# Optimization experiments

Measured on AMD Instinct MI355X. Metric: run time of the kernel, lower is better.

Reference implementation:

```python
import jax, jax.numpy as jnp
import numpy as np

B, F, R, P, C = 2048, 64, 32, 16, 128  # batch, nfeature(dsym), nrole, npattern, dcontext
TAU = 2.0  # posn_attender sharpness


def setup_inputs() -> dict:
    key = jax.random.key(0)
    ks = jax.random.split(key, 16)
    w = lambda k, shape, s=0.05: jax.random.normal(k, shape, jnp.float32) * s
    z = lambda shape: jnp.zeros(shape, jnp.float32)
    return {
        "form": jax.random.normal(ks[0], (B, F, R), jnp.float32),
        "context": jax.random.normal(ks[1], (B, C), jnp.float32),
        "mod_W": w(ks[2], (C, P * 6)), "mod_b": z((P * 6,)),
        "wch_W": w(ks[3], (C, P * F)), "wch_b": z((P * F,)),
        "wdl_W": w(ks[4], (C, P)), "wdl_b": z((P,)),
        "wep_W": w(ks[5], (C, P * 4)), "wep_b": z((P * 4,)),
        "vch_W": w(ks[6], (C, P * F)), "vch_b": z((P * F,)),
        "vep_W": w(ks[7], (C, P * F * 4)), "vep_b": z((P * F * 4,)),
        "wnc_W": w(ks[8], (C, F)), "wnc_b": z((F,)),
        "wnd_W": w(ks[9], (C, 1)), "wnd_b": z((1,)),
        "wne_W": w(ks[10], (C, 1)), "wne_b": z((1,)),
        "m_W": w(ks[11], (3, C, P * F)), "m_Wb": z((3, P * F)),
        "mb_W": w(ks[12], (3, C, P)), "mb_b": z((3, P)),
    }


def _forward(form, context, mod_W, mod_b, wch_W, wch_b, wdl_W, wdl_b,
             wep_W, wep_b, vch_W, vch_b, vep_W, vep_b,
             wnc_W, wnc_b, wnd_W, wnd_b, wne_W, wne_b,
             m_W, m_Wb, mb_W, mb_b):
    nb = form.shape[0]
    lin = lambda W, b: context @ W + b

    # context-conditioned rule weights
    mod = jax.nn.softmax(lin(mod_W, mod_b).reshape(nb, P, 6), axis=-1)
    w_chng = mod[..., 0:1] * lin(wch_W, wch_b).reshape(nb, P, F)
    w_deln = mod[..., 1:2] * lin(wdl_W, wdl_b).reshape(nb, P, 1)
    w_epen = mod[..., 2:] * lin(wep_W, wep_b).reshape(nb, P, 4)
    v_chng = lin(vch_W, vch_b).reshape(nb, P, F)
    v_epen = lin(vep_W, vep_b).reshape(nb, P, F, 4)
    w_nochng = jnp.exp(lin(wnc_W, wnc_b))   # (B, F)
    w_nodeln = jnp.exp(lin(wnd_W, wnd_b))   # (B, 1)
    w_noepen = jnp.exp(lin(wne_W, wne_b))   # (B, 1)

    # Matcher3: trigram (prev, cur, next) feature matching; log-prob summed then exp'd
    prev = jnp.pad(form[:, :, :-1], ((0, 0), (0, 0), (1, 0)))
    nxt = jnp.pad(form[:, :, 1:], ((0, 0), (0, 0), (0, 1)))
    forms3 = jnp.stack([prev, form, nxt], 0)                                   # (3,B,F,R)
    Wk = (jnp.einsum('bc,kcn->kbn', context, m_W) + m_Wb[:, None, :]).reshape(3, nb, P, F)
    bk = jnp.einsum('bc,kcp->kbp', context, mb_W) + mb_b[:, None, :]
    score = jnp.einsum('kbpf,kbfr->kbpr', Wk, forms3) + bk[..., None]
    match = jnp.exp(jnp.sum(jax.nn.log_sigmoid(score), axis=0))                # (B,P,R)

    positions = jnp.arange(R, dtype=form.dtype)

    def posn_attn(posn):  # (B,1) soft position -> (B,R) radial-basis attention
        return jax.nn.softmax(-TAU * (posn - positions[None, :]) ** 2, axis=-1)

    def bind(out, x, attn):  # soft write symbol x at attended role
        a = attn[:, None, :]
        return out * (1.0 - a) + x[:, :, None] * a

    def epen(out, posn, match_i, we_p, ve_p):
        we = match_i * we_p                                                    # (B,P)
        p = jax.nn.sigmoid(jnp.sum(we, 1, keepdims=True) - w_noepen)           # (B,1)
        v = jnp.sum(jax.nn.relu(we)[..., None] * ve_p, 1)                      # (B,F)
        out_ = bind(out, v, posn_attn(posn))
        out = p[..., None] * out_ + (1.0 - p[..., None]) * out
        return out, posn + p

    def step(carry, x):
        out, posn = carry
        sym_i, match_i = x  # (B,F), (B,P)
        # epenthesis before
        out, posn = epen(out, posn, match_i, w_epen[..., 0], v_epen[..., 0])
        # feature change + deletion
        wc = match_i[..., None] * w_chng                                       # (B,P,F)
        p_chng = jax.nn.sigmoid(jnp.sum(wc, 1) - w_nochng)                     # (B,F)
        vc = jnp.sum(jax.nn.relu(wc) * v_chng, 1)                              # (B,F)
        sym = sym_i + p_chng * (vc - sym_i)
        out_ = bind(out, sym, posn_attn(posn))
        wd = match_i[..., None] * w_deln                                       # (B,P,1)
        p_deln = jax.nn.sigmoid(jnp.sum(wd, 1) - w_nodeln)                     # (B,1)
        out = (1.0 - p_deln[..., None]) * out_ + p_deln[..., None] * out
        posn = posn + (1.0 - p_deln)
        # epenthesis after
        out, posn = epen(out, posn, match_i, w_epen[..., 2], v_epen[..., 2])
        return (out, posn), None

    carry0 = (jnp.zeros((nb, F, R), form.dtype), jnp.zeros((nb, 1), form.dtype))
    xs = (jnp.moveaxis(form, 2, 0), jnp.moveaxis(match, 2, 0))
    (out, _), _ = jax.lax.scan(step, carry0, xs)
    return out


def reference(form, context, mod_W, mod_b, wch_W, wch_b, wdl_W, wdl_b,
              wep_W, wep_b, vch_W, vch_b, vep_W, vep_b,
              wnc_W, wnc_b, wnd_W, wnd_b, wne_W, wne_b,
              m_W, m_Wb, mb_W, mb_b):
    return _forward(form, context, mod_W, mod_b, wch_W, wch_b, wdl_W, wdl_b,
                    wep_W, wep_b, vch_W, vch_b, vep_W, vep_b,
                    wnc_W, wnc_b, wnd_W, wnd_b, wne_W, wne_b,
                    m_W, m_Wb, mb_W, mb_b)
```

## Files before the change

kernel.cpp:

```cpp
#include <hip/hip_runtime.h>

#define B_ 2048
#define YS2 7168
#define NTILES 448

typedef unsigned short u16;
typedef unsigned int   u32;
typedef __attribute__((ext_vector_type(2))) float v2f;
typedef __attribute__((ext_vector_type(8))) short bf16x8;
typedef __attribute__((ext_vector_type(4))) float f32x4;

__device__ __forceinline__ float bfu(u16 u) {
    u32 i = ((u32)u) << 16; float f; __builtin_memcpy(&f, &i, 4); return f;
}
__device__ __forceinline__ u16 f2bf(float v) {
    u32 iv; __builtin_memcpy(&iv, &v, 4);
    u32 r = (iv + 0x7fffu + ((iv >> 16) & 1u)) >> 16;
    return (u16)r;
}
__device__ __forceinline__ float sigm(float x) { return 1.f / (1.f + __expf(-x)); }
__device__ __forceinline__ float lsg(float x) {
    return fminf(x, 0.f) - log1pf(__expf(-fabsf(x)));
}

template<bool F32> __device__ __forceinline__ float LD(const void* p, int e) {
    if (F32) return ((const float*)p)[e];
    return bfu(((const u16*)p)[e]);
}
template<bool F32> __device__ __forceinline__ float2 LD2(const void* p, int e) {
    if (F32) { const float* q = (const float*)p; return make_float2(q[e], q[e + 1]); }
    u32 w = ((const u32*)p)[e >> 1];
    u32 lo = w << 16, hi = w & 0xffff0000u; float a, b;
    __builtin_memcpy(&a, &lo, 4); __builtin_memcpy(&b, &hi, 4);
    return make_float2(a, b);
}
template<bool F32> __device__ __forceinline__ float4 LD4(const void* p, int e) {
    if (F32) return ((const float4*)p)[e >> 2];
    uint2 w = ((const uint2*)p)[e >> 2];
    u32 a0 = w.x << 16, a1 = w.x & 0xffff0000u, a2 = w.y << 16, a3 = w.y & 0xffff0000u;
    float f0, f1, f2, f3;
    __builtin_memcpy(&f0, &a0, 4); __builtin_memcpy(&f1, &a1, 4);
    __builtin_memcpy(&f2, &a2, 4); __builtin_memcpy(&f3, &a3, 4);
    return make_float4(f0, f1, f2, f3);
}
template<bool F32> __device__ __forceinline__ void ST(void* p, int e, float v) {
    if (F32) ((float*)p)[e] = v; else ((u16*)p)[e] = f2bf(v);
}

struct Args {
    const void *form, *ctx;
    const void *mod_W, *mod_b, *wch_W, *wch_b, *wdl_W, *wdl_b, *wep_W, *wep_b;
    const void *vch_W, *vch_b, *vep_W, *vep_b;
    const void *wnc_W, *wnc_b, *wnd_W, *wnd_b, *wne_W, *wne_b;
    const void *m_W, *m_Wb, *mb_W, *mb_b;
    void* outp;
};

__device__ __forceinline__ int probe_is_f32(const void* ctx, int t, int* flag_s) {
    if (t == 0) {
        int sane = 0;
        const u16* q = (const u16*)ctx;
        for (int i = 0; i < 64; ++i) {
            u16 u = q[2 * i];
            int ex = (u >> 7) & 0xFF;
            sane += (u == 0 || (ex >= 112 && ex <= 143)) ? 1 : 0;
        }
        *flag_s = (sane < 32) ? 1 : 0;
    }
    __syncthreads();
    return *flag_s;
}

__device__ __forceinline__ void split_bf16(float x, u16& hi, u16& lo) {
    hi = f2bf(x);
    lo = f2bf(x - bfu(hi));
}


template<bool F32>
__device__ void packw_body(int g, const Args& A, u16* Bpack, float* bcat) {
    int l  = g & 63;
    int kb = (g >> 6) & 3;
    int h  = (g >> 8) & 1;
    int T  = g >> 9;
    int n  = T * 16 + (l & 15);
    int k0 = kb * 32 + (l >> 4) * 8;

    const void* p; int off, st;
    if (n < 1024)      { p = A.wch_W; off = n;           st = 1024; }
    else if (n < 2048) { p = A.vch_W; off = n - 1024;    st = 1024; }
    else if (n < 4096) { int i = n - 2048; int col = 4 * (i >> 1) + 2 * (i & 1);
                         p = A.vep_W; off = col;         st = 4096; }
    else               { int i = n - 4096; int kk = i >> 10, j2 = i & 1023;
                         p = A.m_W;  off = kk * 131072 + j2; st = 1024; }

    u16 out[8];
    #pragma unroll
    for (int j = 0; j < 8; ++j) {
        float w = LD<F32>(p, off + (k0 + j) * st);
        u16 whi, wlo; split_bf16(w, whi, wlo);
        out[j] = h ? wlo : whi;
    }
    *(uint4*)(Bpack + (size_t)g * 8) = *(const uint4*)out;

    if (h == 0 && kb == 0 && l < 16) {
        float bb;
        if (n < 1024)      bb = LD<F32>(A.wch_b, n);
        else if (n < 2048) bb = LD<F32>(A.vch_b, n - 1024);
        else if (n < 4096) { int i = n - 2048; bb = LD<F32>(A.vep_b, 4 * (i >> 1) + 2 * (i & 1)); }
        else               { int i = n - 4096; bb = LD<F32>(A.m_Wb, (i >> 10) * 1024 + (i & 1023)); }
        bcat[n] = bb;
    }
}

__global__ __launch_bounds__(256) void packw_kernel(Args A, u16* Bpack, float* bcat) {
    __shared__ int dt_s;
    const int t = threadIdx.x;
    int isf32 = probe_is_f32(A.ctx, t, &dt_s);
    int g = blockIdx.x * 256 + t;
    if (isf32) packw_body<true>(g, A, Bpack, bcat);
    else       packw_body<false>(g, A, Bpack, bcat);
}

template<bool F32>
__device__ void packa_body(int g, const Args& A, u16* Apack) {
    int l  = g & 63;
    int kb = (g >> 6) & 3;
    int h  = (g >> 8) & 1;
    int M  = g >> 9;
    int m  = M * 16 + (l & 15);
    int k0 = kb * 32 + (l >> 4) * 8;

    u16 out[8];
    float4 x = LD4<F32>(A.ctx, m * 128 + k0);
    float4 y = LD4<F32>(A.ctx, m * 128 + k0 + 4);
    float v[8] = {x.x, x.y, x.z, x.w, y.x, y.y, y.z, y.w};
    #pragma unroll
    for (int j = 0; j < 8; ++j) {
        u16 whi, wlo; split_bf16(v[j], whi, wlo);
        out[j] = h ? wlo : whi;
    }
    *(uint4*)(Apack + (size_t)g * 8) = *(const uint4*)out;
}

__global__ __launch_bounds__(256) void packa_kernel(Args A, u16* Apack) {
    __shared__ int dt_s;
    const int t = threadIdx.x;
    int isf32 = probe_is_f32(A.ctx, t, &dt_s);
    int g = blockIdx.x * 256 + t;
    if (isf32) packa_body<true>(g, A, Apack);
    else       packa_body<false>(g, A, Apack);
}

__global__ __launch_bounds__(256) void gemm_mfma_kernel(
    const u16* __restrict__ Apack, const u16* __restrict__ Bpack,
    const float* __restrict__ bcat, float* __restrict__ Y) {
    __shared__ __align__(16) u16 Astage[4096];

    const int t  = threadIdx.x;
    const int l  = t & 63;
    const int w  = t >> 6;
    const int Mt = blockIdx.x & 127;
    const int nb = blockIdx.x >> 7;

    {
        const uint4* Ap4 = (const uint4*)(Apack + (size_t)Mt * 4096);
        uint4* As4 = (uint4*)Astage;
        As4[t] = Ap4[t];
        As4[t + 256] = Ap4[t + 256];
    }
    __syncthreads();

    bf16x8 ahi[4], alo[4];
    #pragma unroll
    for (int kb = 0; kb < 4; ++kb) {
        ahi[kb] = *(const bf16x8*)(Astage + ((0 * 4 + kb) * 64 + l) * 8);
        alo[kb] = *(const bf16x8*)(Astage + ((1 * 4 + kb) * 64 + l) * 8);
    }

    const int Tbase = nb * 16 + w * 4;
    const int row0  = Mt * 16 + (l >> 4) * 4;
    const int ncol  = l & 15;

    #pragma unroll
    for (int T = 0; T < 4; ++T) {
        const u16* Bb = Bpack + (size_t)(Tbase + T) * 4096;
        bf16x8 bhi[4], blo[4];
        #pragma unroll
        for (int kb = 0; kb < 4; ++kb) {
            bhi[kb] = *(const bf16x8*)(Bb + ((0 * 4 + kb) * 64 + l) * 8);
            blo[kb] = *(const bf16x8*)(Bb + ((1 * 4 + kb) * 64 + l) * 8);
        }
        f32x4 d = {0.f, 0.f, 0.f, 0.f};
        #pragma unroll
        for (int kb = 0; kb < 4; ++kb) {
            d = __builtin_amdgcn_mfma_f32_16x16x32_bf16(ahi[kb], bhi[kb], d, 0, 0, 0);
            d = __builtin_amdgcn_mfma_f32_16x16x32_bf16(ahi[kb], blo[kb], d, 0, 0, 0);
            d = __builtin_amdgcn_mfma_f32_16x16x32_bf16(alo[kb], bhi[kb], d, 0, 0, 0);
        }
        int n = (Tbase + T) * 16 + ncol;
        float bv = bcat[n];
        #pragma unroll
        for (int i = 0; i < 4; ++i) {
            Y[(size_t)(row0 + i) * YS2 + n] = d[i] + bv;
        }
    }
}

struct __align__(16) ScanSmem {
    float U[6144];
    float V[3072];
    float match_s[512];
    float wnc_s[64];
    float wep0_s[16], wep2_s[16], wdl_s[16];
    float coef_s[96];
    float sc_s[2];
};

template<bool F32>
__device__ void scan_body(ScanSmem& S, int t, int b, const Args& A, const float* __restrict__ Y) {
    float* Wk_s   = S.U;
    float* bk_s   = S.U + 3072;
    float* modl   = S.U + 3120;
    float* form_s = S.U + 3312;
    float* ctx_s  = S.U + 5424;
    float* xtab   = S.U;
    float* wch_s  = S.V;
    float* vch_s  = S.V + 1024;
    float* rlI    = S.V + 2048;
    float* gtab   = S.V;

    const float* Yr = Y + (size_t)b * YS2;
    const float4* Y4 = (const float4*)Yr;

    const int f_own = t & 63;
    const int fq    = t >> 6;

    const float2* vep2p = (const float2*)(Yr + 2048);
    v2f vepf[16];
    #pragma unroll
    for (int p = 0; p < 16; ++p) {
        float2 v = vep2p[p * 64 + f_own];
        vepf[p].x = v.x; vepf[p].y = v.y;
    }

    {
        int e0 = b * 2048 + t * 8;
        float4 x = LD4<F32>(A.form, e0);
        float4 y = LD4<F32>(A.form, e0 + 4);
        int f = t >> 2, r0 = (t & 3) * 8;
        float* dst = form_s + f * 33 + r0;
        dst[0] = x.x; dst[1] = x.y; dst[2] = x.z; dst[3] = x.w;
        dst[4] = y.x; dst[5] = y.y; dst[6] = y.z; dst[7] = y.w;
    }
    if (t < 32) {
        float4 v = LD4<F32>(A.ctx, b * 128 + 4 * t);
        *(float4*)&ctx_s[4 * t] = v;
    }
    for (int i = t; i < 768; i += 256) ((float4*)Wk_s)[i] = Y4[1024 + i];
    ((float4*)wch_s)[t] = Y4[t];
    ((float4*)vch_s)[t] = Y4[256 + t];
    __syncthreads();

    if (t < 96) {
        float a = LD<F32>(A.mod_b, t);
        for (int c = 0; c < 128; ++c) a += ctx_s[c] * LD<F32>(A.mod_W, c * 96 + t);
        modl[t] = a;
    } else if (t < 144) {
        int i = t - 96; int k = i >> 4, p = i & 15;
        float a = LD<F32>(A.mb_b, k * 16 + p);
        for (int c = 0; c < 128; ++c) a += ctx_s[c] * LD<F32>(A.mb_W, (k * 128 + c) * 16 + p);
        bk_s[i] = a;
    } else if (t < 208) {
        int f = t - 144;
        float a = LD<F32>(A.wnc_b, f);
        for (int c = 0; c < 128; ++c) a += ctx_s[c] * LD<F32>(A.wnc_W, c * 64 + f);
        S.wnc_s[f] = __expf(a);
    } else if (t < 224) {
        int p = t - 208;
        float a0 = LD<F32>(A.wep_b, 4 * p), a2 = LD<F32>(A.wep_b, 4 * p + 2);
        for (int c = 0; c < 128; ++c) {
            float cv = ctx_s[c];
            a0 += cv * LD<F32>(A.wep_W, c * 64 + 4 * p);
            a2 += cv * LD<F32>(A.wep_W, c * 64 + 4 * p + 2);
        }
        S.wep0_s[p] = a0; S.wep2_s[p] = a2;
    } else if (t < 240) {
        int p = t - 224;
        float a = LD<F32>(A.wdl_b, p);
        for (int c = 0; c < 128; ++c) a += ctx_s[c] * LD<F32>(A.wdl_W, c * 16 + p);
        S.wdl_s[p] = a;
    } else if (t < 242) {
        const void* W  = (t == 240) ? A.wnd_W : A.wne_W;
        const void* bb = (t == 240) ? A.wnd_b : A.wne_b;
        float a = LD<F32>(bb, 0);
        for (int c = 0; c < 128; ++c) a += ctx_s[c] * LD<F32>(W, c);
        S.sc_s[t - 240] = __expf(a);
    }
    __syncthreads();

    if (t < 16) {
        float v[6]; float mx = -1e30f;
        #pragma unroll
        for (int j = 0; j < 6; ++j) { v[j] = modl[t * 6 + j]; mx = fmaxf(mx, v[j]); }
        float s = 0.f;
        #pragma unroll
        for (int j = 0; j < 6; ++j) { v[j] = __expf(v[j] - mx); s += v[j]; }
        float inv = 1.f / s;
        #pragma unroll
        for (int j = 0; j < 6; ++j) modl[t * 6 + j] = v[j] * inv;
    }
    __syncthreads();

    if (t < 16) {
        S.wep0_s[t] *= modl[t * 6 + 2];
        S.wep2_s[t] *= modl[t * 6 + 4];
        S.wdl_s[t]  *= modl[t * 6 + 1];
    }
    for (int i = t; i < 1024; i += 256) wch_s[i] *= modl[(i >> 6) * 6];

    const int my_r = t & 31;
    #pragma unroll 1
    for (int it = 0; it < 2; ++it) {
        int idx = t + 256 * it;
        int p = idx >> 5, r = idx & 31;
        float s0 = bk_s[p], s1 = bk_s[16 + p], s2 = bk_s[32 + p];
        const float4* w0 = (const float4*)(Wk_s + p * 64);
        const float4* w1 = (const float4*)(Wk_s + (16 + p) * 64);
        const float4* w2 = (const float4*)(Wk_s + (32 + p) * 64);
        for (int f4 = 0; f4 < 16; ++f4) {
            float a0[4], a1[4], a2[4];
            *(float4*)a0 = w0[f4]; *(float4*)a1 = w1[f4]; *(float4*)a2 = w2[f4];
            #pragma unroll
            for (int j = 0; j < 4; ++j) {
                int f = f4 * 4 + j;
                float f0 = form_s[f * 33 + r];
                float fm = __shfl_up(f0, 1, 32);   if (r == 0)  fm = 0.f;
                float fp = __shfl_down(f0, 1, 32); if (r == 31) fp = 0.f;
                s0 += a0[j] * fm; s1 += a1[j] * f0; s2 += a2[j] * fp;
            }
        }
        S.match_s[p * 32 + r] = __expf(lsg(s0) + lsg(s1) + lsg(s2));
    }
    __syncthreads();

    if (t < 96) {
        int sub = t >> 5, r = t & 31;
        const float* w = (sub == 0) ? S.wep0_s : (sub == 1) ? S.wdl_s : S.wep2_s;
        float s = 0.f;
        for (int p = 0; p < 16; ++p) s += S.match_s[p * 32 + r] * w[p];
        float cf;
        if (sub == 1) cf = 1.f - sigm(s - S.sc_s[0]);
        else          cf = sigm(s - S.sc_s[1]);
        S.coef_s[sub * 32 + r] = cf;
    }
    for (int i = t; i < 512; i += 256) {
        int p = i >> 5, r = i & 31;
        float m = S.match_s[p * 32 + r];
        rlI[2 * i]     = fmaxf(m * S.wep0_s[p], 0.f);
        rlI[2 * i + 1] = fmaxf(m * S.wep2_s[p], 0.f);
    }
    float wchf[16], vchf[16];
    #pragma unroll
    for (int p = 0; p < 16; ++p) {
        wchf[p] = wch_s[p * 64 + f_own];
        vchf[p] = vch_s[p * 64 + f_own];
    }
    const float wncf = S.wnc_s[f_own];
    float si_r[8];
    #pragma unroll
    for (int j = 0; j < 8; ++j) si_r[j] = form_s[f_own * 33 + fq * 8 + j];
    __syncthreads();

    #pragma unroll 1
    for (int j = 0; j < 8; ++j) {
        int rs = fq * 8 + j;
        v2f v02; v02.x = 0.f; v02.y = 0.f;
        float sum = 0.f, vs1 = 0.f;
        const v2f* rlp = (const v2f*)(rlI + 2 * rs);
        #pragma unroll
        for (int p = 0; p < 16; ++p) {
            v2f rl = rlp[p * 32];
            v02 += rl * vepf[p];
            float m = S.match_s[p * 32 + rs];
            float wc = m * wchf[p];
            sum += wc;
            vs1 += fmaxf(wc, 0.f) * vchf[p];
        }
        float pch = sigm(sum - wncf);
        float si  = si_r[j];
        xtab[0 * 2048 + rs * 64 + f_own] = v02.x;
        xtab[1 * 2048 + rs * 64 + f_own] = si + pch * (vs1 - si);
        xtab[2 * 2048 + rs * 64 + f_own] = v02.y;
    }
    __syncthreads();

    float* ck_s  = S.match_s;
    float* pos_s = S.match_s + 128;
    if (t < 96) ck_s[t] = S.coef_s[(t % 3) * 32 + (t / 3)];
    __syncthreads();
    if (t < 64) {
        float a = ck_s[t];
        float a0 = a;
        #pragma unroll
        for (int d = 1; d < 64; d <<= 1) { float v = __shfl_up(a, d, 64); if (t >= d) a += v; }
        pos_s[t] = a - a0;
        float carry = __shfl(a, 63, 64);
        float b2 = (t < 32) ? ck_s[64 + t] : 0.f;
        float c2 = b2;
        #pragma unroll
        for (int d = 1; d < 32; d <<= 1) { float v = __shfl_up(c2, d, 32); if ((t & 31) >= d) c2 += v; }
        if (t < 32) pos_s[64 + t] = carry + c2 - b2;
    }
    __syncthreads();

    #pragma unroll 1
    for (int i = 0; i < 12; ++i) {
        int idx = t + 256 * i;
        int k = idx >> 5, r = idx & 31;
        float posn = pos_s[k];
        float pc = fminf(posn, 31.f);
        float ci = floorf(pc + 0.5f);
        float dmin = posn - ci;
        float dd = posn - (float)r;
        float eo = __expf(-2.f * (dd * dd - dmin * dmin));
        float Z = eo;
        Z += __shfl_xor(Z, 1, 32);
        Z += __shfl_xor(Z, 2, 32);
        Z += __shfl_xor(Z, 4, 32);
        Z += __shfl_xor(Z, 8, 32);
        Z += __shfl_xor(Z, 16, 32);
        gtab[idx] = ck_s[k] * eo / Z;
    }
    __syncthreads();

    const int fgrp = t >> 5;
    v2f o01, o23, o45, o67;
    o01 = 0.f; o23 = 0.f; o45 = 0.f; o67 = 0.f;
    #pragma unroll 1
    for (int rs = 0; rs < 32; ++rs) {
        #pragma unroll
        for (int sub = 0; sub < 3; ++sub) {
            float g = gtab[(rs * 3 + sub) * 32 + my_r];
            v2f gv; gv.x = g; gv.y = g;
            const float4* xb = (const float4*)(xtab + sub * 2048 + rs * 64 + fgrp * 8);
            float4 xa = xb[0], xc = xb[1];
            v2f x01, x23, x45, x67;
            x01.x = xa.x; x01.y = xa.y; x23.x = xa.z; x23.y = xa.w;
            x45.x = xc.x; x45.y = xc.y; x67.x = xc.z; x67.y = xc.w;
            o01 += gv * (x01 - o01);
            o23 += gv * (x23 - o23);
            o45 += gv * (x45 - o45);
            o67 += gv * (x67 - o67);
        }
    }

    float oreg[8] = {o01.x, o01.y, o23.x, o23.y, o45.x, o45.y, o67.x, o67.y};
    #pragma unroll
    for (int i = 0; i < 8; ++i) {
        ST<F32>(A.outp, b * 2048 + (fgrp * 8 + i) * 32 + my_r, oreg[i]);
    }
}

__global__ __launch_bounds__(256) void scan_kernel(Args A, const float* Y) {
    __shared__ ScanSmem S;
    __shared__ int dt_s;
    const int t = threadIdx.x, b = blockIdx.x;
    int isf32 = probe_is_f32(A.ctx, t, &dt_s);
    if (isf32) scan_body<true>(S, t, b, A, Y);
    else       scan_body<false>(S, t, b, A, Y);
}

struct Smem {
    float U[6144];
    float form_s[64 * 33];
    float match_s[512];
    float wch_s[1024];
    float vch_s[1024];
    float vep0_s[1024];
    float vep2_s[1024];
    float wep0_s[16], wep2_s[16], wdl_s[16];
    float wnc_s[64];
    float sc_s[2];
    float ssum_s[96];
};

template<bool F32>
__device__ void mono_body(Smem& S, int t, int b, const Args& A) {
    float* c_s  = S.U;
    float* modl = S.U + 128;
    float* Wk_s = S.U + 224;
    float* bk_s = S.U + 3344;
    float* xtab = S.U;

    if (t < 128) c_s[t] = LD<F32>(A.ctx, b * 128 + t);
    {
        int e0 = b * 2048 + t * 8;
        float4 x = LD4<F32>(A.form, e0);
        float4 y = LD4<F32>(A.form, e0 + 4);
        int f = t >> 2, r0 = (t & 3) * 8;
        float* dst = S.form_s + f * 33 + r0;
        dst[0] = x.x; dst[1] = x.y; dst[2] = x.z; dst[3] = x.w;
        dst[4] = y.x; dst[5] = y.y; dst[6] = y.z; dst[7] = y.w;
    }
    __syncthreads();
    if (t < 96) {
        float a = LD<F32>(A.mod_b, t);
        for (int cc = 0; cc < 128; ++cc) a += c_s[cc] * LD<F32>(A.mod_W, cc * 96 + t);
        modl[t] = a;
    }
    __syncthreads();
    if (t < 16) {
        float v[6]; float mx = -1e30f;
        #pragma unroll
        for (int j = 0; j < 6; ++j) { v[j] = modl[t * 6 + j]; mx = fmaxf(mx, v[j]); }
        float s = 0.f;
        #pragma unroll
        for (int j = 0; j < 6; ++j) { v[j] = __expf(v[j] - mx); s += v[j]; }
        float inv = 1.f / s;
        #pragma unroll
        for (int j = 0; j < 6; ++j) modl[t * 6 + j] = v[j] * inv;
    }
    __syncthreads();
    for (int j = t; j < 512; j += 256) {
        int n0 = j * 2;
        float2 bb = LD2<F32>(A.wch_b, n0);
        float a0 = bb.x, a1 = bb.y;
        for (int cc = 0; cc < 128; ++cc) {
            float2 w = LD2<F32>(A.wch_W, cc * 1024 + n0); float cv = c_s[cc];
            a0 += cv * w.x; a1 += cv * w.y;
        }
        int p = n0 >> 6; float sc = modl[p * 6 + 0];
        S.wch_s[n0] = sc * a0; S.wch_s[n0 + 1] = sc * a1;
    }
    for (int j = t; j < 512; j += 256) {
        int n0 = j * 2;
        float2 bb = LD2<F32>(A.vch_b, n0);
        float a0 = bb.x, a1 = bb.y;
        for (int cc = 0; cc < 128; ++cc) {
            float2 w = LD2<F32>(A.vch_W, cc * 1024 + n0); float cv = c_s[cc];
            a0 += cv * w.x; a1 += cv * w.y;
        }
        S.vch_s[n0] = a0; S.vch_s[n0 + 1] = a1;
    }
    for (int u = t; u < 1024; u += 256) {
        int n0 = u * 4;
        float4 bb = LD4<F32>(A.vep_b, n0);
        float a0 = bb.x, a2 = bb.z;
        for (int cc = 0; cc < 128; ++cc) {
            float4 w = LD4<F32>(A.vep_W, cc * 4096 + n0); float cv = c_s[cc];
            a0 += cv * w.x; a2 += cv * w.z;
        }
        S.vep0_s[u] = a0; S.vep2_s[u] = a2;
    }
    for (int j = t; j < 1536; j += 256) {
        int k  = j >> 9;
        int jj = j & 511;
        int n0 = jj * 2;
        float2 bb = LD2<F32>(A.m_Wb, k * 1024 + n0);
        float a0 = bb.x, a1 = bb.y;
        for (int cc = 0; cc < 128; ++cc) {
            float2 w = LD2<F32>(A.m_W, (k * 128 + cc) * 1024 + n0); float cv = c_s[cc];
            a0 += cv * w.x; a1 += cv * w.y;
        }
        int p = n0 >> 6, f = n0 & 63;
        Wk_s[(k * 16 + p) * 65 + f]     = a0;
        Wk_s[(k * 16 + p) * 65 + f + 1] = a1;
    }
    if (t < 16) {
        int n0 = t * 4;
        float4 bb = LD4<F32>(A.wep_b, n0);
        float a0 = bb.x, a2 = bb.z;
        for (int cc = 0; cc < 128; ++cc) {
            float4 w = LD4<F32>(A.wep_W, cc * 64 + n0); float cv = c_s[cc];
            a0 += cv * w.x; a2 += cv * w.z;
        }
        S.wep0_s[t] = modl[t * 6 + 2] * a0;
        S.wep2_s[t] = modl[t * 6 + 4] * a2;
    } else if (t < 32) {
        int p = t - 16;
        float a = LD<F32>(A.wdl_b, p);
        for (int cc = 0; cc < 128; ++cc) a += c_s[cc] * LD<F32>(A.wdl_W, cc * 16 + p);
        S.wdl_s[p] = modl[p * 6 + 1] * a;
    } else if (t < 96) {
        int f = t - 32;
        float a = LD<F32>(A.wnc_b, f);
        for (int cc = 0; cc < 128; ++cc) a += c_s[cc] * LD<F32>(A.wnc_W, cc * 64 + f);
        S.wnc_s[f] = __expf(a);
    } else if (t < 98) {
        const void* W  = (t == 96) ? A.wnd_W : A.wne_W;
        const void* bb = (t == 96) ? A.wnd_b : A.wne_b;
        float a = LD<F32>(bb, 0);
        for (int cc = 0; cc < 128; ++cc) a += c_s[cc] * LD<F32>(W, cc);
        S.sc_s[t - 96] = __expf(a);
    } else if (t < 146) {
        int i = t - 98;
        int k = i >> 4, p = i & 15;
        float a = LD<F32>(A.mb_b, k * 16 + p);
        for (int cc = 0; cc < 128; ++cc) a += c_s[cc] * LD<F32>(A.mb_W, (k * 128 + cc) * 16 + p);
        bk_s[i] = a;
    }
    __syncthreads();
    for (int idx = t; idx < 512; idx += 256) {
        int p = idx >> 5, r = idx & 31;
        float s0 = bk_s[p], s1 = bk_s[16 + p], s2 = bk_s[32 + p];
        const float* w0 = Wk_s + p * 65;
        const float* w1 = Wk_s + (16 + p) * 65;
        const float* w2 = Wk_s + (32 + p) * 65;
        for (int f = 0; f < 64; ++f) {
            const float* fr = S.form_s + f * 33 + r;
            float fm1 = (r > 0)  ? fr[-1] : 0.f;
            float f0  = fr[0];
            float fp1 = (r < 31) ? fr[1]  : 0.f;
            s0 += w0[f] * fm1; s1 += w1[f] * f0; s2 += w2[f] * fp1;
        }
        S.match_s[p * 32 + r] = __expf(lsg(s0) + lsg(s1) + lsg(s2));
    }
    __syncthreads();
    if (t < 96) {
        int which = t >> 5, r = t & 31;
        const float* w = (which == 0) ? S.wep0_s : (which == 1) ? S.wep2_s : S.wdl_s;
        float s = 0.f;
        for (int p = 0; p < 16; ++p) s += S.match_s[p * 32 + r] * w[p];
        S.ssum_s[which * 32 + r] = s;
    }
    #pragma unroll 1
    for (int q = 0; q < 24; ++q) {
        int idx = t + 256 * q;
        int sub = idx >> 11;
        int rs  = (idx >> 6) & 31;
        int f   = idx & 63;
        float x;
        if (sub == 1) {
            float sum = 0.f, vs = 0.f;
            for (int p = 0; p < 16; ++p) {
                float wc = S.match_s[p * 32 + rs] * S.wch_s[p * 64 + f];
                sum += wc;
                vs  += fmaxf(wc, 0.f) * S.vch_s[p * 64 + f];
            }
            float pch = sigm(sum - S.wnc_s[f]);
            float si  = S.form_s[f * 33 + rs];
            x = si + pch * (vs - si);
        } else {
            const float* wep = (sub == 0) ? S.wep0_s : S.wep2_s;
            const float* vep = (sub == 0) ? S.vep0_s : S.vep2_s;
            float vs = 0.f;
            for (int p = 0; p < 16; ++p) {
                float w = S.match_s[p * 32 + rs] * wep[p];
                vs += fmaxf(w, 0.f) * vep[p * 64 + f];
            }
            x = vs;
        }
        xtab[idx] = x;
    }
    __syncthreads();
    const int my_r = t & 31;
    const int fgrp = t >> 5;
    float oreg[8];
    #pragma unroll
    for (int i = 0; i < 8; ++i) oreg[i] = 0.f;
    float posn = 0.f;
    const float wnd1v = S.sc_s[0];
    const float wne1v = S.sc_s[1];
    for (int rs = 0; rs < 32; ++rs) {
        #pragma unroll
        for (int sub = 0; sub < 3; ++sub) {
            float coef;
            if (sub == 1) coef = 1.f - sigm(S.ssum_s[64 + rs] - wnd1v);
            else          coef = sigm(S.ssum_s[(sub & 2) * 16 + rs] - wne1v);
            float pc = fminf(posn, 31.f);
            int ci = (int)(pc + 0.5f);
            int lo = ci - 4; if (lo < 0)  lo = 0;
            int hi = ci + 4; if (hi > 31) hi = 31;
            float dmin = posn - (float)ci;
            float mx = -2.f * dmin * dmin;
            float Z = 0.f, eo = 0.f;
            for (int r = lo; r <= hi; ++r) {
                float d = posn - (float)r;
                float e = __expf(-2.f * d * d - mx);
                Z += e;
                if (r == my_r) eo = e;
            }
            float g = coef * eo / Z;
            const float* xb = xtab + (sub * 2048 + rs * 64 + fgrp * 8);
            #pragma unroll
            for (int i = 0; i < 8; ++i) oreg[i] += g * (xb[i] - oreg[i]);
            posn += coef;
        }
    }
    #pragma unroll
    for (int i = 0; i < 8; ++i) {
        ST<F32>(A.outp, b * 2048 + (fgrp * 8 + i) * 32 + my_r, oreg[i]);
    }
}

__global__ __launch_bounds__(256) void phon_mono(Args A) {
    __shared__ Smem S;
    __shared__ int dt_s;
    const int t = threadIdx.x, b = blockIdx.x;
    int isf32 = probe_is_f32(A.ctx, t, &dt_s);
    if (isf32) mono_body<true>(S, t, b, A);
    else       mono_body<false>(S, t, b, A);
}

extern "C" void kernel_launch(void* const* d_in, const int* in_sizes, int n_in,
                              void* d_out, int out_size, void* d_ws, size_t ws_size,
                              hipStream_t stream) {
    Args A;
    A.form  = d_in[0];  A.ctx   = d_in[1];
    A.mod_W = d_in[2];  A.mod_b = d_in[3];
    A.wch_W = d_in[4];  A.wch_b = d_in[5];
    A.wdl_W = d_in[6];  A.wdl_b = d_in[7];
    A.wep_W = d_in[8];  A.wep_b = d_in[9];
    A.vch_W = d_in[10]; A.vch_b = d_in[11];
    A.vep_W = d_in[12]; A.vep_b = d_in[13];
    A.wnc_W = d_in[14]; A.wnc_b = d_in[15];
    A.wnd_W = d_in[16]; A.wnd_b = d_in[17];
    A.wne_W = d_in[18]; A.wne_b = d_in[19];
    A.m_W   = d_in[20]; A.m_Wb  = d_in[21];
    A.mb_W  = d_in[22]; A.mb_b  = d_in[23];
    A.outp  = d_out;

    const size_t yElems  = (size_t)B_ * YS2;
    const size_t bpElems = (size_t)NTILES * 4096;
    const size_t apElems = (size_t)128 * 4096;
    const size_t need = yElems * 4 + (bpElems + apElems) * 2 + YS2 * 4;
    if (ws_size >= need) {
        float* Y     = (float*)d_ws;
        u16*   Bpack = (u16*)(Y + yElems);
        u16*   Apack = Bpack + bpElems;
        float* bcat  = (float*)(Apack + apElems);
        packw_kernel<<<896, 256, 0, stream>>>(A, Bpack, bcat);
        packa_kernel<<<256, 256, 0, stream>>>(A, Apack);
        gemm_mfma_kernel<<<3584, 256, 0, stream>>>(Apack, Bpack, bcat, Y);
        scan_kernel<<<B_, 256, 0, stream>>>(A, Y);
    } else {
        phon_mono<<<B_, 256, 0, stream>>>(A);
    }
}
```

Before: 265.9 us.

## Fold small context projections into MFMA GEMM and drop A-packing kernel

The small context projections (mod, mb, wep, wdl, wnc, wnd, wne) are appended as extra zero-padded output columns of the big split-bf16 MFMA GEMM, so the scan kernel reads them from Y instead of running per-block 128-long serial dot products. The separate packa kernel is removed: the GEMM now stages fp32 context in LDS and splits it into hi/lo bf16 in-register. packw now writes the hi and lo halves from one thread, halving its grid. This removes one launch and per-batch serial work, at the cost of a wider Y buffer and redundant A splitting in every GEMM block.

```diff
diff --git a/kernel.cpp b/kernel.cpp
--- a/kernel.cpp
+++ b/kernel.cpp
@@ -1,8 +1,8 @@
 #include <hip/hip_runtime.h>
 
 #define B_ 2048
-#define YS2 7168
-#define NTILES 448
+#define YS3 7440
+#define NT  465
 
 typedef unsigned short u16;
 typedef unsigned int   u32;
@@ -81,36 +81,38 @@
 __device__ void packw_body(int g, const Args& A, u16* Bpack, float* bcat) {
     int l  = g & 63;
     int kb = (g >> 6) & 3;
-    int h  = (g >> 8) & 1;
-    int T  = g >> 9;
+    int T  = g >> 8;
     int n  = T * 16 + (l & 15);
     int k0 = kb * 32 + (l >> 4) * 8;
 
-    const void* p; int off, st;
-    if (n < 1024)      { p = A.wch_W; off = n;           st = 1024; }
-    else if (n < 2048) { p = A.vch_W; off = n - 1024;    st = 1024; }
+    const void* p = A.wch_W; int off = 0, st = 0, zero = 0; float bb = 0.f;
+    if (n < 1024)      { off = n; st = 1024; bb = LD<F32>(A.wch_b, n); }
+    else if (n < 2048) { int j = n - 1024; p = A.vch_W; off = j; st = 1024; bb = LD<F32>(A.vch_b, j); }
     else if (n < 4096) { int i = n - 2048; int col = 4 * (i >> 1) + 2 * (i & 1);
-                         p = A.vep_W; off = col;         st = 4096; }
-    else               { int i = n - 4096; int kk = i >> 10, j2 = i & 1023;
-                         p = A.m_W;  off = kk * 131072 + j2; st = 1024; }
-
-    u16 out[8];
+                         p = A.vep_W; off = col; st = 4096; bb = LD<F32>(A.vep_b, col); }
+    else if (n < 7168) { int i = n - 4096; int kk = i >> 10, j = i & 1023;
+                         p = A.m_W; off = kk * 131072 + j; st = 1024; bb = LD<F32>(A.m_Wb, kk * 1024 + j); }
+    else if (n < 7264) { int m = n - 7168; p = A.mod_W; off = m; st = 96; bb = LD<F32>(A.mod_b, m); }
+    else if (n < 7312) { int i = n - 7264; int k = i >> 4, pp = i & 15;
+                         p = A.mb_W; off = k * 2048 + pp; st = 16; bb = LD<F32>(A.mb_b, k * 16 + pp); }
+    else if (n < 7344) { int i = n - 7312; int col = 4 * (i >> 1) + 2 * (i & 1);
+                         p = A.wep_W; off = col; st = 64; bb = LD<F32>(A.wep_b, col); }
+    else if (n < 7360) { int j = n - 7344; p = A.wdl_W; off = j; st = 16; bb = LD<F32>(A.wdl_b, j); }
+    else if (n < 7424) { int j = n - 7360; p = A.wnc_W; off = j; st = 64; bb = LD<F32>(A.wnc_b, j); }
+    else if (n == 7424){ p = A.wnd_W; off = 0; st = 1; bb = LD<F32>(A.wnd_b, 0); }
+    else if (n == 7425){ p = A.wne_W; off = 0; st = 1; bb = LD<F32>(A.wne_b, 0); }
+    else zero = 1;
+
+    u16 hi[8], lo[8];
     #pragma unroll
     for (int j = 0; j < 8; ++j) {
         float w = LD<F32>(p, off + (k0 + j) * st);
-        u16 whi, wlo; split_bf16(w, whi, wlo);
-        out[j] = h ? wlo : whi;
-    }
-    *(uint4*)(Bpack + (size_t)g * 8) = *(const uint4*)out;
-
-    if (h == 0 && kb == 0 && l < 16) {
-        float bb;
-        if (n < 1024)      bb = LD<F32>(A.wch_b, n);
-        else if (n < 2048) bb = LD<F32>(A.vch_b, n - 1024);
-        else if (n < 4096) { int i = n - 2048; bb = LD<F32>(A.vep_b, 4 * (i >> 1) + 2 * (i & 1)); }
-        else               { int i = n - 4096; bb = LD<F32>(A.m_Wb, (i >> 10) * 1024 + (i & 1023)); }
-        bcat[n] = bb;
-    }
+        if (zero) w = 0.f;
+        split_bf16(w, hi[j], lo[j]);
+    }
+    *(uint4*)(Bpack + ((size_t)T * 512 + kb * 64 + l) * 8)       = *(const uint4*)hi;
+    *(uint4*)(Bpack + ((size_t)T * 512 + 256 + kb * 64 + l) * 8) = *(const uint4*)lo;
+    if (kb == 0 && l < 16) bcat[n] = zero ? 0.f : bb;
 }
 
 __global__ __launch_bounds__(256) void packw_kernel(Args A, u16* Bpack, float* bcat) {
@@ -123,59 +125,35 @@
 }
 
 template<bool F32>
-__device__ void packa_body(int g, const Args& A, u16* Apack) {
-    int l  = g & 63;
-    int kb = (g >> 6) & 3;
-    int h  = (g >> 8) & 1;
-    int M  = g >> 9;
-    int m  = M * 16 + (l & 15);
-    int k0 = kb * 32 + (l >> 4) * 8;
-
-    u16 out[8];
-    float4 x = LD4<F32>(A.ctx, m * 128 + k0);
-    float4 y = LD4<F32>(A.ctx, m * 128 + k0 + 4);
-    float v[8] = {x.x, x.y, x.z, x.w, y.x, y.y, y.z, y.w};
-    #pragma unroll
-    for (int j = 0; j < 8; ++j) {
-        u16 whi, wlo; split_bf16(v[j], whi, wlo);
-        out[j] = h ? wlo : whi;
-    }
-    *(uint4*)(Apack + (size_t)g * 8) = *(const uint4*)out;
-}
-
-__global__ __launch_bounds__(256) void packa_kernel(Args A, u16* Apack) {
-    __shared__ int dt_s;
-    const int t = threadIdx.x;
-    int isf32 = probe_is_f32(A.ctx, t, &dt_s);
-    int g = blockIdx.x * 256 + t;
-    if (isf32) packa_body<true>(g, A, Apack);
-    else       packa_body<false>(g, A, Apack);
-}
-
-__global__ __launch_bounds__(256) void gemm_mfma_kernel(
-    const u16* __restrict__ Apack, const u16* __restrict__ Bpack,
-    const float* __restrict__ bcat, float* __restrict__ Y) {
-    __shared__ __align__(16) u16 Astage[4096];
-
-    const int t  = threadIdx.x;
+__device__ void gemm_mfma_body(float* As, int t, int blk, const void* __restrict__ ctx,
+                               const u16* __restrict__ Bpack,
+                               const float* __restrict__ bcat, float* __restrict__ Y) {
     const int l  = t & 63;
     const int w  = t >> 6;
-    const int Mt = blockIdx.x & 127;
-    const int nb = blockIdx.x >> 7;
+    const int Mt = blk & 127;
+    const int nb = blk >> 7;
 
     {
-        const uint4* Ap4 = (const uint4*)(Apack + (size_t)Mt * 4096);
-        uint4* As4 = (uint4*)Astage;
-        As4[t] = Ap4[t];
-        As4[t + 256] = Ap4[t + 256];
+        int row = t >> 4, c0 = (t & 15) * 8;
+        float4 x = LD4<F32>(ctx, (Mt * 16 + row) * 128 + c0);
+        float4 y = LD4<F32>(ctx, (Mt * 16 + row) * 128 + c0 + 4);
+        *(float4*)&As[row * 132 + c0]     = x;
+        *(float4*)&As[row * 132 + c0 + 4] = y;
     }
     __syncthreads();
 
     bf16x8 ahi[4], alo[4];
+    const int m = l & 15;
     #pragma unroll
     for (int kb = 0; kb < 4; ++kb) {
-        ahi[kb] = *(const bf16x8*)(Astage + ((0 * 4 + kb) * 64 + l) * 8);
-        alo[kb] = *(const bf16x8*)(Astage + ((1 * 4 + kb) * 64 + l) * 8);
+        int k0 = kb * 32 + (l >> 4) * 8;
+        const float* ap = &As[m * 132 + k0];
+        #pragma unroll
+        for (int j = 0; j < 8; ++j) {
+            u16 hi, lo; split_bf16(ap[j], hi, lo);
+            ahi[kb][j] = (short)hi;
+            alo[kb][j] = (short)lo;
+        }
     }
 
     const int Tbase = nb * 16 + w * 4;
@@ -184,12 +162,14 @@
 
     #pragma unroll
     for (int T = 0; T < 4; ++T) {
-        const u16* Bb = Bpack + (size_t)(Tbase + T) * 4096;
+        int Tt = Tbase + T;
+        if (Tt >= NT) break;
+        const u16* Bb = Bpack + (size_t)Tt * 4096;
         bf16x8 bhi[4], blo[4];
         #pragma unroll
         for (int kb = 0; kb < 4; ++kb) {
-            bhi[kb] = *(const bf16x8*)(Bb + ((0 * 4 + kb) * 64 + l) * 8);
-            blo[kb] = *(const bf16x8*)(Bb + ((1 * 4 + kb) * 64 + l) * 8);
+            bhi[kb] = *(const bf16x8*)(Bb + ((kb) * 64 + l) * 8);
+            blo[kb] = *(const bf16x8*)(Bb + ((4 + kb) * 64 + l) * 8);
         }
         f32x4 d = {0.f, 0.f, 0.f, 0.f};
         #pragma unroll
@@ -198,13 +178,23 @@
             d = __builtin_amdgcn_mfma_f32_16x16x32_bf16(ahi[kb], blo[kb], d, 0, 0, 0);
             d = __builtin_amdgcn_mfma_f32_16x16x32_bf16(alo[kb], bhi[kb], d, 0, 0, 0);
         }
-        int n = (Tbase + T) * 16 + ncol;
+        int n = Tt * 16 + ncol;
         float bv = bcat[n];
         #pragma unroll
         for (int i = 0; i < 4; ++i) {
-            Y[(size_t)(row0 + i) * YS2 + n] = d[i] + bv;
-        }
-    }
+            Y[(size_t)(row0 + i) * YS3 + n] = d[i] + bv;
+        }
+    }
+}
+
+__global__ __launch_bounds__(256) void gemm_mfma_kernel(Args A, const u16* Bpack,
+                                                        const float* bcat, float* Y) {
+    __shared__ float As[16 * 132];
+    __shared__ int dt_s;
+    const int t = threadIdx.x, blk = blockIdx.x;
+    int isf32 = probe_is_f32(A.ctx, t, &dt_s);
+    if (isf32) gemm_mfma_body<true>(As, t, blk, A.ctx, Bpack, bcat, Y);
+    else       gemm_mfma_body<false>(As, t, blk, A.ctx, Bpack, bcat, Y);
 }
 
 struct __align__(16) ScanSmem {
@@ -223,14 +213,13 @@
     float* bk_s   = S.U + 3072;
     float* modl   = S.U + 3120;
     float* form_s = S.U + 3312;
-    float* ctx_s  = S.U + 5424;
     float* xtab   = S.U;
     float* wch_s  = S.V;
     float* vch_s  = S.V + 1024;
     float* rlI    = S.V + 2048;
     float* gtab   = S.V;
 
-    const float* Yr = Y + (size_t)b * YS2;
+    const float* Yr = Y + (size_t)b * YS3;
     const float4* Y4 = (const float4*)Yr;
 
     const int f_own = t & 63;
@@ -253,49 +242,19 @@
         dst[0] = x.x; dst[1] = x.y; dst[2] = x.z; dst[3] = x.w;
         dst[4] = y.x; dst[5] = y.y; dst[6] = y.z; dst[7] = y.w;
     }
-    if (t < 32) {
-        float4 v = LD4<F32>(A.ctx, b * 128 + 4 * t);
-        *(float4*)&ctx_s[4 * t] = v;
-    }
     for (int i = t; i < 768; i += 256) ((float4*)Wk_s)[i] = Y4[1024 + i];
+    if (t < 12) ((float4*)bk_s)[t] = Y4[1816 + t];
+    if (t < 24) ((float4*)modl)[t] = Y4[1792 + t];
     ((float4*)wch_s)[t] = Y4[t];
     ((float4*)vch_s)[t] = Y4[256 + t];
-    __syncthreads();
-
-    if (t < 96) {
-        float a = LD<F32>(A.mod_b, t);
-        for (int c = 0; c < 128; ++c) a += ctx_s[c] * LD<F32>(A.mod_W, c * 96 + t);
-        modl[t] = a;
-    } else if (t < 144) {
-        int i = t - 96; int k = i >> 4, p = i & 15;
-        float a = LD<F32>(A.mb_b, k * 16 + p);
-        for (int c = 0; c < 128; ++c) a += ctx_s[c] * LD<F32>(A.mb_W, (k * 128 + c) * 16 + p);
-        bk_s[i] = a;
-    } else if (t < 208) {
-        int f = t - 144;
-        float a = LD<F32>(A.wnc_b, f);
-        for (int c = 0; c < 128; ++c) a += ctx_s[c] * LD<F32>(A.wnc_W, c * 64 + f);
-        S.wnc_s[f] = __expf(a);
-    } else if (t < 224) {
-        int p = t - 208;
-        float a0 = LD<F32>(A.wep_b, 4 * p), a2 = LD<F32>(A.wep_b, 4 * p + 2);
-        for (int c = 0; c < 128; ++c) {
-            float cv = ctx_s[c];
-            a0 += cv * LD<F32>(A.wep_W, c * 64 + 4 * p);
-            a2 += cv * LD<F32>(A.wep_W, c * 64 + 4 * p + 2);
-        }
-        S.wep0_s[p] = a0; S.wep2_s[p] = a2;
-    } else if (t < 240) {
-        int p = t - 224;
-        float a = LD<F32>(A.wdl_b, p);
-        for (int c = 0; c < 128; ++c) a += ctx_s[c] * LD<F32>(A.wdl_W, c * 16 + p);
-        S.wdl_s[p] = a;
-    } else if (t < 242) {
-        const void* W  = (t == 240) ? A.wnd_W : A.wne_W;
-        const void* bb = (t == 240) ? A.wnd_b : A.wne_b;
-        float a = LD<F32>(bb, 0);
-        for (int c = 0; c < 128; ++c) a += ctx_s[c] * LD<F32>(W, c);
-        S.sc_s[t - 240] = __expf(a);
+    if (t < 16) {
+        S.wep0_s[t] = Yr[7312 + 2 * t];
+        S.wep2_s[t] = Yr[7312 + 2 * t + 1];
+        S.wdl_s[t]  = Yr[7344 + t];
+    } else if (t >= 32 && t < 96) {
+        S.wnc_s[t - 32] = __expf(Yr[7360 + (t - 32)]);
+    } else if (t >= 96 && t < 98) {
+        S.sc_s[t - 96] = __expf(Yr[7424 + (t - 96)]);
     }
     __syncthreads();
 
@@ -721,18 +680,15 @@
     A.mb_W  = d_in[22]; A.mb_b  = d_in[23];
     A.outp  = d_out;
 
-    const size_t yElems  = (size_t)B_ * YS2;
-    const size_t bpElems = (size_t)NTILES * 4096;
-    const size_t apElems = (size_t)128 * 4096;
-    const size_t need = yElems * 4 + (bpElems + apElems) * 2 + YS2 * 4;
+    const size_t yElems  = (size_t)B_ * YS3;
+    const size_t bpElems = (size_t)NT * 4096;
+    const size_t need = yElems * 4 + bpElems * 2 + (size_t)YS3 * 4;
     if (ws_size >= need) {
         float* Y     = (float*)d_ws;
         u16*   Bpack = (u16*)(Y + yElems);
-        u16*   Apack = Bpack + bpElems;
-        float* bcat  = (float*)(Apack + apElems);
-        packw_kernel<<<896, 256, 0, stream>>>(A, Bpack, bcat);
-        packa_kernel<<<256, 256, 0, stream>>>(A, Apack);
-        gemm_mfma_kernel<<<3584, 256, 0, stream>>>(Apack, Bpack, bcat, Y);
+        float* bcat  = (float*)(Bpack + bpElems);
+        packw_kernel<<<NT, 256, 0, stream>>>(A, Bpack, bcat);
+        gemm_mfma_kernel<<<30 * 128, 256, 0, stream>>>(A, Bpack, bcat, Y);
         scan_kernel<<<B_, 256, 0, stream>>>(A, Y);
     } else {
         phon_mono<<<B_, 256, 0, stream>>>(A);
```

After: 243.8 us. 8.3% less time.
